# Kernel optimization log

Measured on AMD Instinct MI355X. Metric: run time of the kernel, lower is better.

## Reference

```python
import jax
import jax.numpy as jnp
from jax import lax
import numpy as np

N_PRE = 1024
N_POST = 2048
SEQ_LEN = 4096
DECAY = 0.9   # leak factor per timestep
V_TH = 1.0    # firing threshold


def setup_inputs() -> dict:
    key = jax.random.key(0)
    k1, k2 = jax.random.split(key)
    stim = (jax.random.uniform(k1, (N_PRE, SEQ_LEN), dtype=jnp.float32) < 0.1).astype(jnp.float32)  # sparse input spikes
    weights = jax.random.normal(k2, (N_POST, N_PRE), dtype=jnp.float32) * 0.05
    return {"stim": stim, "weights": weights}


def reference(stim, weights):
    # Synaptic currents for all timesteps at once: cal_post_input(stim[:, i]) == weights @ stim[:, i]
    currents = jnp.einsum("np,pt->nt", weights, stim)  # [n_post, T]

    def lif_step(v, i_t):
        # leaky integrate
        v = v * DECAY + i_t
        # fire
        s = (v >= V_TH).astype(v.dtype)
        # reset to 0 where spiked
        v_next = jnp.where(s > 0, jnp.zeros_like(v), v)
        return v_next, (s, v_next)

    v0 = jnp.zeros((N_POST,), dtype=stim.dtype)
    _, (spikes_t, v_t) = lax.scan(lif_step, v0, currents.T)  # scanned over T
    # transpose back to [n_post, T] to match spike_times / v buffers
    return spikes_t.T, v_t.T
```

## Files before the change

kernel.cpp:

```cpp
#include <hip/hip_runtime.h>

#define N_PRE 1024
#define N_POST 2048
#define SEQ_LEN 4096

#define KSPLIT 512

__device__ __forceinline__ float opaque(float x) {
  asm volatile("" : "+v"(x));
  return x;
}

__device__ __forceinline__ float load_dyn(const void* p, size_t idx, bool isbf) {
  if (isbf) {
    const unsigned short b = ((const unsigned short*)p)[idx];
    return __uint_as_float(((unsigned int)b) << 16);
  }
  return ((const float*)p)[idx];
}

__device__ __forceinline__ int sniff_flags(const void* W, const void* S, int tid,
                                           int* flags_sh) {
  if (tid < 64) {
    const unsigned short* uw = (const unsigned short*)W;
    const float f = fabsf(__uint_as_float(((unsigned int)uw[tid * 2]) << 16));
    const bool big = !(f < 64.f);
    const unsigned long long wb = __ballot(big);
    const unsigned short* us = (const unsigned short*)S;
    int hit = 0;
    for (int j = 0; j < 64; ++j) hit |= (us[tid * 128 + 2 * j] == 0x3F80u) ? 1 : 0;
    const unsigned long long sb = __ballot(hit != 0);
    if (tid == 0) *flags_sh = ((wb == 0ull) ? 1 : 0) | ((sb != 0ull) ? 2 : 0);
  }
  __syncthreads();
  return *flags_sh;
}

__global__ __launch_bounds__(256, 2) void snn_gemm_v2(const void* __restrict__ W,
                                                      const void* __restrict__ S,
                                                      float* __restrict__ C,
                                                      int t0, int chunkT) {
  __shared__ float As[16][132];
  __shared__ float Bs[16][132];
  __shared__ int flags_sh;
  const int tid = threadIdx.x;
  const int fl = sniff_flags(W, S, tid, &flags_sh);
  const bool w_bf = (fl & 1) != 0;
  const bool s_bf = (fl & 2) != 0;

  const int tx = tid & 15;
  const int ty = tid >> 4;
  const int m0 = blockIdx.y * 128;
  const int nl0 = blockIdx.x * 128;

  float acc0[8][8] = {{0.f}};
  float acc1[8][8] = {{0.f}};

  int k0 = 0;
#define KTILE_BODY(ACC)                                                          \
  {                                                                              \
                        \
    if (!w_bf) {                                                                 \
      const float* Wf = (const float*)W;                                         \
      const int row = tid >> 2;                                                  \
      const int c4 = (tid & 3) * 4;                                              \
      _Pragma("unroll") for (int h = 0; h < 2; ++h) {                            \
        const int m = row + 64 * h;                                              \
        const float4 va =                                                        \
            *(const float4*)&Wf[(size_t)(m0 + m) * N_PRE + k0 + c4];             \
        As[c4 + 0][m] = va.x; As[c4 + 1][m] = va.y;                              \
        As[c4 + 2][m] = va.z; As[c4 + 3][m] = va.w;                              \
      }                                                                          \
    } else {                                                                     \
      _Pragma("unroll") for (int e = 0; e < 8; ++e) {                            \
        const int idx = tid * 8 + e;                                             \
        const int m = idx >> 4, c = idx & 15;                                    \
        As[c][m] = load_dyn(W, (size_t)(m0 + m) * N_PRE + k0 + c, true);         \
      }                                                                          \
    }                                                                            \
                    \
    {                                                                            \
      const int r = tid >> 4;                                                    \
      const int c8 = (tid & 15) * 8;                                             \
      if (s_bf) {                                                                \
        const unsigned short* Sb = (const unsigned short*)S;                     \
        const uint4 u =                                                          \
            *(const uint4*)&Sb[(size_t)(k0 + r) * SEQ_LEN + t0 + nl0 + c8];      \
        Bs[r][c8 + 0] = __uint_as_float(u.x << 16);                              \
        Bs[r][c8 + 1] = __uint_as_float(u.x & 0xFFFF0000u);                      \
        Bs[r][c8 + 2] = __uint_as_float(u.y << 16);                              \
        Bs[r][c8 + 3] = __uint_as_float(u.y & 0xFFFF0000u);                      \
        Bs[r][c8 + 4] = __uint_as_float(u.z << 16);                              \
        Bs[r][c8 + 5] = __uint_as_float(u.z & 0xFFFF0000u);                      \
        Bs[r][c8 + 6] = __uint_as_float(u.w << 16);                              \
        Bs[r][c8 + 7] = __uint_as_float(u.w & 0xFFFF0000u);                      \
      } else {                                                                   \
        const float* Sf = (const float*)S;                                       \
        const size_t base = (size_t)(k0 + r) * SEQ_LEN + t0 + nl0 + c8;          \
        *(float4*)&Bs[r][c8] = *(const float4*)&Sf[base];                        \
        *(float4*)&Bs[r][c8 + 4] = *(const float4*)&Sf[base + 4];                \
      }                                                                          \
    }                                                                            \
    __syncthreads();                                                             \
    _Pragma("unroll") for (int k = 0; k < 16; ++k) {                             \
      float a[8], b[8];                                                          \
      *(float4*)&a[0] = *(const float4*)&As[k][ty * 8];                          \
      *(float4*)&a[4] = *(const float4*)&As[k][ty * 8 + 4];                      \
      *(float4*)&b[0] = *(const float4*)&Bs[k][tx * 8];                          \
      *(float4*)&b[4] = *(const float4*)&Bs[k][tx * 8 + 4];                      \
      _Pragma("unroll") for (int i = 0; i < 8; ++i)                              \
          _Pragma("unroll") for (int j = 0; j < 8; ++j)                          \
              ACC[i][j] += a[i] * b[j];       \
    }                                                                            \
    __syncthreads();                                                             \
  }

  for (; k0 < KSPLIT; k0 += 16) KTILE_BODY(acc0)
  for (; k0 < N_PRE; k0 += 16) KTILE_BODY(acc1)
#undef KTILE_BODY

#pragma unroll
  for (int i = 0; i < 8; ++i) {
    float r[8];
#pragma unroll
    for (int j = 0; j < 8; ++j) r[j] = acc0[i][j] + acc1[i][j];
    float* dst = &C[(size_t)(m0 + ty * 8 + i) * chunkT + nl0 + tx * 8];
    *(float4*)&dst[0] = make_float4(r[0], r[1], r[2], r[3]);
    *(float4*)&dst[4] = make_float4(r[4], r[5], r[6], r[7]);
  }
}

#define SROWS 16
#define STT 64
#define SPAD 68
__global__ __launch_bounds__(256) void snn_scan_v2(const float* __restrict__ cur,
                                                   float* __restrict__ spk,
                                                   float* __restrict__ vout,
                                                   float* __restrict__ v_carry,
                                                   int t0, int chunkT, int first) {
  __shared__ float c_t[2][SROWS][SPAD];
  __shared__ float s_t[SROWS][SPAD];
  __shared__ float v_t[SROWS][SPAD];
  const int tid = threadIdx.x;
  const int n0 = blockIdx.x * SROWS;
  const int row = tid >> 4;
  const int c4 = (tid & 15) * 4;

  float v = 0.0f;
  if (tid < SROWS && !first) v = v_carry[n0 + tid];

  const int ntiles = chunkT / STT;
  *(float4*)&c_t[0][row][c4] =
      *(const float4*)&cur[(size_t)(n0 + row) * chunkT + 0 + c4];
  __syncthreads();

  for (int it = 0; it < ntiles; ++it) {
    const int buf = it & 1;
    if (it + 1 < ntiles) {
      *(float4*)&c_t[buf ^ 1][row][c4] =
          *(const float4*)&cur[(size_t)(n0 + row) * chunkT + (it + 1) * STT + c4];
    }
    if (tid < SROWS) {
#pragma unroll
      for (int g = 0; g < STT / 16; ++g) {
        float c[16], s[16], vv[16];
        *(float4*)&c[0] = *(const float4*)&c_t[buf][tid][g * 16];
        *(float4*)&c[4] = *(const float4*)&c_t[buf][tid][g * 16 + 4];
        *(float4*)&c[8] = *(const float4*)&c_t[buf][tid][g * 16 + 8];
        *(float4*)&c[12] = *(const float4*)&c_t[buf][tid][g * 16 + 12];
#pragma unroll
        for (int k = 0; k < 16; ++k) {
          const float leak = opaque(v * 0.9f);
          v = leak + c[k];
          const bool fired = (v >= 1.0f);
          s[k] = fired ? 1.0f : 0.0f;
          v = fired ? 0.0f : v;
          vv[k] = v;
        }
        *(float4*)&s_t[tid][g * 16] = make_float4(s[0], s[1], s[2], s[3]);
        *(float4*)&s_t[tid][g * 16 + 4] = make_float4(s[4], s[5], s[6], s[7]);
        *(float4*)&s_t[tid][g * 16 + 8] = make_float4(s[8], s[9], s[10], s[11]);
        *(float4*)&s_t[tid][g * 16 + 12] = make_float4(s[12], s[13], s[14], s[15]);
        *(float4*)&v_t[tid][g * 16] = make_float4(vv[0], vv[1], vv[2], vv[3]);
        *(float4*)&v_t[tid][g * 16 + 4] = make_float4(vv[4], vv[5], vv[6], vv[7]);
        *(float4*)&v_t[tid][g * 16 + 8] = make_float4(vv[8], vv[9], vv[10], vv[11]);
        *(float4*)&v_t[tid][g * 16 + 12] = make_float4(vv[12], vv[13], vv[14], vv[15]);
      }
    }
    __syncthreads();
    {
      const size_t g = (size_t)(n0 + row) * SEQ_LEN + t0 + it * STT + c4;
      *(float4*)&spk[g] = *(const float4*)&s_t[row][c4];
      *(float4*)&vout[g] = *(const float4*)&v_t[row][c4];
    }
    __syncthreads();
  }

  if (tid < SROWS) v_carry[n0 + tid] = v;
}

__global__ __launch_bounds__(256) void snn_fused_blis(const void* __restrict__ W,
                                                      const void* __restrict__ S,
                                                      float* __restrict__ spk,
                                                      float* __restrict__ vout) {
  __shared__ float As[16][68];
  __shared__ float Bs[16][68];
  __shared__ float Ct[64][65];
  __shared__ float vsh[64];
  __shared__ int flags_sh;
  const int tid = threadIdx.x;
  const int fl = sniff_flags(W, S, tid, &flags_sh);
  const bool w_bf = (fl & 1) != 0;
  const bool s_bf = (fl & 2) != 0;

  const int tx = tid & 15;
  const int ty = tid >> 4;
  const int m0 = blockIdx.x * 64;
  if (tid < 64) vsh[tid] = 0.0f;

  for (int t0 = 0; t0 < SEQ_LEN; t0 += 64) {
    float acc0[4][4] = {{0.f}};
    float acc1[4][4] = {{0.f}};
    int k0 = 0;
#define FUSED_SEGMENT(ACC, KEND)                                                 \
    for (; k0 < (KEND); k0 += 16) {                                              \
      {                                                                          \
        const int r = tid >> 4, c = tid & 15;                                    \
        _Pragma("unroll") for (int j = 0; j < 4; ++j)                            \
            As[c][r + 16 * j] =                                                  \
                load_dyn(W, (size_t)(m0 + r + 16 * j) * N_PRE + k0 + c, w_bf);   \
      }                                                                          \
      {                                                                          \
        const int r = tid >> 6, c = tid & 63;                                    \
        _Pragma("unroll") for (int j = 0; j < 4; ++j)                            \
            Bs[r + 4 * j][c] =                                                   \
                load_dyn(S, (size_t)(k0 + r + 4 * j) * SEQ_LEN + t0 + c, s_bf);  \
      }                                                                          \
      __syncthreads();                                                           \
      _Pragma("unroll") for (int k = 0; k < 16; ++k) {                           \
        _Pragma("unroll") for (int i = 0; i < 4; ++i)                            \
            _Pragma("unroll") for (int j = 0; j < 4; ++j)                        \
                ACC[i][j] += As[k][ty * 4 + i] * Bs[k][tx * 4 + j];              \
      }                                                                          \
      __syncthreads();                                                           \
    }

    FUSED_SEGMENT(acc0, KSPLIT)
    FUSED_SEGMENT(acc1, N_PRE)
#undef FUSED_SEGMENT

#pragma unroll
    for (int i = 0; i < 4; ++i)
#pragma unroll
      for (int j = 0; j < 4; ++j) Ct[ty * 4 + i][tx * 4 + j] = acc0[i][j] + acc1[i][j];
    __syncthreads();
    if (tid < 64) {
      float v = vsh[tid];
#pragma unroll
      for (int k = 0; k < 64; ++k) {
        const float leak = opaque(v * 0.9f);
        v = leak + Ct[tid][k];
        const bool fired = (v >= 1.0f);
        const size_t g = (size_t)(m0 + tid) * SEQ_LEN + t0 + k;
        spk[g] = fired ? 1.0f : 0.0f;
        v = fired ? 0.0f : v;
        vout[g] = v;
      }
      vsh[tid] = v;
    }
    __syncthreads();
  }
}

extern "C" void kernel_launch(void* const* d_in, const int* in_sizes, int n_in,
                              void* d_out, int out_size, void* d_ws, size_t ws_size,
                              hipStream_t stream) {
  const void* stim = d_in[0];
  const void* weights = d_in[1];
  if (n_in >= 2 && in_sizes[0] == N_POST * N_PRE && in_sizes[1] == N_PRE * SEQ_LEN) {
    weights = d_in[0];
    stim = d_in[1];
  }

  float* spk = (float*)d_out;
  float* vout = spk + (size_t)N_POST * SEQ_LEN;

  const size_t carry_bytes = (size_t)N_POST * sizeof(float);
  float* v_carry = nullptr;
  size_t avail = 0;
  if (ws_size > carry_bytes + 8) {
    const size_t coff = (ws_size - carry_bytes) & ~(size_t)15;
    v_carry = (float*)((char*)d_ws + coff);
    avail = coff;
  }
  int chunkT = (int)((avail / ((size_t)N_POST * sizeof(float))) / 128 * 128);
  if (chunkT > SEQ_LEN) chunkT = SEQ_LEN;

  if (chunkT >= 128) {
    float* cur = (float*)d_ws;
    for (int t0 = 0; t0 < SEQ_LEN; t0 += chunkT) {
      const int ct = (SEQ_LEN - t0 < chunkT) ? (SEQ_LEN - t0) : chunkT;
      snn_gemm_v2<<<dim3(ct / 128, N_POST / 128), dim3(256), 0, stream>>>(weights, stim, cur,
                                                                          t0, ct);
      snn_scan_v2<<<dim3(N_POST / SROWS), dim3(256), 0, stream>>>(cur, spk, vout, v_carry,
                                                                  t0, ct, t0 == 0);
    }
  } else {
    snn_fused_blis<<<dim3(N_POST / 64), dim3(256), 0, stream>>>(weights, stim, spk, vout);
  }
}
```

Baseline: 410.9 us.

## Double-buffer GEMM tiles via register prefetch and shrink scan to single-wave blocks

The GEMM now keeps two LDS buffers and prefetches the next K-tile into registers while computing on the current one, which removes one barrier per tile. The B-fragment column mapping changes to strided halves to ease LDS bank conflicts. The scan kernel runs as a single 64-thread wave, so its __syncthreads calls can be dropped. Its recurrence is reordered to take the leak multiply off the critical dependency chain. Risks include more register pressure in the GEMM and reliance on implicit wave-level ordering of LDS accesses in the barrier-free scan.

Result: slower. 1.637 ms (+298.4%).

```diff
diff --git a/kernel.cpp b/kernel.cpp
--- a/kernel.cpp
+++ b/kernel.cpp
@@ -7,7 +7,7 @@
 #define KSPLIT 512
 
 __device__ __forceinline__ float opaque(float x) {
-  asm volatile("" : "+v"(x));
+  asm("" : "+v"(x));
   return x;
 }
 
@@ -36,12 +36,12 @@
   return *flags_sh;
 }
 
-__global__ __launch_bounds__(256, 2) void snn_gemm_v2(const void* __restrict__ W,
+__global__ __launch_bounds__(256, 2) void snn_gemm_v3(const void* __restrict__ W,
                                                       const void* __restrict__ S,
                                                       float* __restrict__ C,
                                                       int t0, int chunkT) {
-  __shared__ float As[16][132];
-  __shared__ float Bs[16][132];
+  __shared__ float As[2][16][132];
+  __shared__ float Bs[2][16][132];
   __shared__ int flags_sh;
   const int tid = threadIdx.x;
   const int fl = sniff_flags(W, S, tid, &flags_sh);
@@ -53,116 +53,157 @@
   const int m0 = blockIdx.y * 128;
   const int nl0 = blockIdx.x * 128;
 
+  const int arow = tid >> 2;
+  const int ac4 = (tid & 3) * 4;
+  const int br = tid >> 4;
+  const int bc8 = (tid & 15) * 8;
+
   float acc0[8][8] = {{0.f}};
   float acc1[8][8] = {{0.f}};
-
-  int k0 = 0;
-#define KTILE_BODY(ACC)                                                          \
+  float4 aR0, aR1;
+  uint4 bRa, bRb;
+
+#define GLOAD(KT)                                                                \
   {                                                                              \
-                        \
+    const int k0 = (KT) * 16;                                                    \
     if (!w_bf) {                                                                 \
       const float* Wf = (const float*)W;                                         \
-      const int row = tid >> 2;                                                  \
-      const int c4 = (tid & 3) * 4;                                              \
-      _Pragma("unroll") for (int h = 0; h < 2; ++h) {                            \
-        const int m = row + 64 * h;                                              \
-        const float4 va =                                                        \
-            *(const float4*)&Wf[(size_t)(m0 + m) * N_PRE + k0 + c4];             \
-        As[c4 + 0][m] = va.x; As[c4 + 1][m] = va.y;                              \
-        As[c4 + 2][m] = va.z; As[c4 + 3][m] = va.w;                              \
-      }                                                                          \
+      aR0 = *(const float4*)&Wf[(size_t)(m0 + arow) * N_PRE + k0 + ac4];         \
+      aR1 = *(const float4*)&Wf[(size_t)(m0 + arow + 64) * N_PRE + k0 + ac4];    \
+    }                                                                            \
+    if (s_bf) {                                                                  \
+      const unsigned short* Sb = (const unsigned short*)S;                       \
+      bRa = *(const uint4*)&Sb[(size_t)(k0 + br) * SEQ_LEN + t0 + nl0 + bc8];    \
     } else {                                                                     \
+      const float* Sf = (const float*)S;                                         \
+      const size_t base = (size_t)(k0 + br) * SEQ_LEN + t0 + nl0 + bc8;          \
+      bRa = *(const uint4*)&Sf[base];                                            \
+      bRb = *(const uint4*)&Sf[base + 4];                                        \
+    }                                                                            \
+  }
+
+#define LSTORE(BUF, KT)                                                          \
+  {                                                                              \
+    if (!w_bf) {                                                                 \
+      As[BUF][ac4 + 0][arow] = aR0.x; As[BUF][ac4 + 1][arow] = aR0.y;            \
+      As[BUF][ac4 + 2][arow] = aR0.z; As[BUF][ac4 + 3][arow] = aR0.w;            \
+      As[BUF][ac4 + 0][arow + 64] = aR1.x; As[BUF][ac4 + 1][arow + 64] = aR1.y;  \
+      As[BUF][ac4 + 2][arow + 64] = aR1.z; As[BUF][ac4 + 3][arow + 64] = aR1.w;  \
+    } else {                                                                     \
+      const int k0 = (KT) * 16;                                                  \
       _Pragma("unroll") for (int e = 0; e < 8; ++e) {                            \
         const int idx = tid * 8 + e;                                             \
         const int m = idx >> 4, c = idx & 15;                                    \
-        As[c][m] = load_dyn(W, (size_t)(m0 + m) * N_PRE + k0 + c, true);         \
+        As[BUF][c][m] = load_dyn(W, (size_t)(m0 + m) * N_PRE + k0 + c, true);    \
       }                                                                          \
     }                                                                            \
-                    \
-    {                                                                            \
-      const int r = tid >> 4;                                                    \
-      const int c8 = (tid & 15) * 8;                                             \
-      if (s_bf) {                                                                \
-        const unsigned short* Sb = (const unsigned short*)S;                     \
-        const uint4 u =                                                          \
-            *(const uint4*)&Sb[(size_t)(k0 + r) * SEQ_LEN + t0 + nl0 + c8];      \
-        Bs[r][c8 + 0] = __uint_as_float(u.x << 16);                              \
-        Bs[r][c8 + 1] = __uint_as_float(u.x & 0xFFFF0000u);                      \
-        Bs[r][c8 + 2] = __uint_as_float(u.y << 16);                              \
-        Bs[r][c8 + 3] = __uint_as_float(u.y & 0xFFFF0000u);                      \
-        Bs[r][c8 + 4] = __uint_as_float(u.z << 16);                              \
-        Bs[r][c8 + 5] = __uint_as_float(u.z & 0xFFFF0000u);                      \
-        Bs[r][c8 + 6] = __uint_as_float(u.w << 16);                              \
-        Bs[r][c8 + 7] = __uint_as_float(u.w & 0xFFFF0000u);                      \
-      } else {                                                                   \
-        const float* Sf = (const float*)S;                                       \
-        const size_t base = (size_t)(k0 + r) * SEQ_LEN + t0 + nl0 + c8;          \
-        *(float4*)&Bs[r][c8] = *(const float4*)&Sf[base];                        \
-        *(float4*)&Bs[r][c8 + 4] = *(const float4*)&Sf[base + 4];                \
-      }                                                                          \
-    }                                                                            \
-    __syncthreads();                                                             \
+    if (s_bf) {                                                                  \
+      float4 f0, f1;                                                             \
+      f0.x = __uint_as_float(bRa.x << 16);                                       \
+      f0.y = __uint_as_float(bRa.x & 0xFFFF0000u);                               \
+      f0.z = __uint_as_float(bRa.y << 16);                                       \
+      f0.w = __uint_as_float(bRa.y & 0xFFFF0000u);                               \
+      f1.x = __uint_as_float(bRa.z << 16);                                       \
+      f1.y = __uint_as_float(bRa.z & 0xFFFF0000u);                               \
+      f1.z = __uint_as_float(bRa.w << 16);                                       \
+      f1.w = __uint_as_float(bRa.w & 0xFFFF0000u);                               \
+      *(float4*)&Bs[BUF][br][bc8] = f0;                                          \
+      *(float4*)&Bs[BUF][br][bc8 + 4] = f1;                                      \
+    } else {                                                                     \
+      *(uint4*)&Bs[BUF][br][bc8] = bRa;                                          \
+      *(uint4*)&Bs[BUF][br][bc8 + 4] = bRb;                                      \
+    }                                                                            \
+  }
+
+#define COMPUTE(BUF, ACC)                                                        \
+  {                                                                              \
     _Pragma("unroll") for (int k = 0; k < 16; ++k) {                             \
       float a[8], b[8];                                                          \
-      *(float4*)&a[0] = *(const float4*)&As[k][ty * 8];                          \
-      *(float4*)&a[4] = *(const float4*)&As[k][ty * 8 + 4];                      \
-      *(float4*)&b[0] = *(const float4*)&Bs[k][tx * 8];                          \
-      *(float4*)&b[4] = *(const float4*)&Bs[k][tx * 8 + 4];                      \
+      *(float4*)&a[0] = *(const float4*)&As[BUF][k][ty * 8];                     \
+      *(float4*)&a[4] = *(const float4*)&As[BUF][k][ty * 8 + 4];                 \
+      *(float4*)&b[0] = *(const float4*)&Bs[BUF][k][tx * 4];        \
+      *(float4*)&b[4] = *(const float4*)&Bs[BUF][k][64 + tx * 4];   \
       _Pragma("unroll") for (int i = 0; i < 8; ++i)                              \
           _Pragma("unroll") for (int j = 0; j < 8; ++j)                          \
               ACC[i][j] += a[i] * b[j];       \
     }                                                                            \
+  }
+
+  GLOAD(0)
+  LSTORE(0, 0)
+  __syncthreads();
+
+  int kt = 0;
+#define STEP(ACC)                                                                \
+  {                                                                              \
+    const int buf = kt & 1;                                                      \
+    if (kt + 1 < 64) GLOAD(kt + 1)                                               \
+    COMPUTE(buf, ACC)                                                            \
+    if (kt + 1 < 64) LSTORE(buf ^ 1, kt + 1)                                     \
     __syncthreads();                                                             \
-  }
-
-  for (; k0 < KSPLIT; k0 += 16) KTILE_BODY(acc0)
-  for (; k0 < N_PRE; k0 += 16) KTILE_BODY(acc1)
-#undef KTILE_BODY
+    ++kt;                                                                        \
+  }
+
+  for (int i = 0; i < 32; ++i) STEP(acc0)
+  for (int i = 0; i < 32; ++i) STEP(acc1)
+#undef STEP
+#undef COMPUTE
+#undef LSTORE
+#undef GLOAD
 
 #pragma unroll
   for (int i = 0; i < 8; ++i) {
-    float r[8];
-#pragma unroll
-    for (int j = 0; j < 8; ++j) r[j] = acc0[i][j] + acc1[i][j];
-    float* dst = &C[(size_t)(m0 + ty * 8 + i) * chunkT + nl0 + tx * 8];
-    *(float4*)&dst[0] = make_float4(r[0], r[1], r[2], r[3]);
-    *(float4*)&dst[4] = make_float4(r[4], r[5], r[6], r[7]);
-  }
-}
-
-#define SROWS 16
+    float4 r0, r1;
+    r0.x = acc0[i][0] + acc1[i][0]; r0.y = acc0[i][1] + acc1[i][1];
+    r0.z = acc0[i][2] + acc1[i][2]; r0.w = acc0[i][3] + acc1[i][3];
+    r1.x = acc0[i][4] + acc1[i][4]; r1.y = acc0[i][5] + acc1[i][5];
+    r1.z = acc0[i][6] + acc1[i][6]; r1.w = acc0[i][7] + acc1[i][7];
+    float* dst = &C[(size_t)(m0 + ty * 8 + i) * chunkT + nl0 + tx * 4];
+    *(float4*)&dst[0] = r0;
+    *(float4*)&dst[64] = r1;
+  }
+}
+
 #define STT 64
-#define SPAD 68
-__global__ __launch_bounds__(256) void snn_scan_v2(const float* __restrict__ cur,
-                                                   float* __restrict__ spk,
-                                                   float* __restrict__ vout,
-                                                   float* __restrict__ v_carry,
-                                                   int t0, int chunkT, int first) {
-  __shared__ float c_t[2][SROWS][SPAD];
-  __shared__ float s_t[SROWS][SPAD];
-  __shared__ float v_t[SROWS][SPAD];
+__global__ __launch_bounds__(64) void snn_scan_v3(const float* __restrict__ cur,
+                                                  float* __restrict__ spk,
+                                                  float* __restrict__ vout,
+                                                  float* __restrict__ v_carry,
+                                                  int t0, int chunkT, int first) {
+  __shared__ float c_t[2][16][STT + 4];
+  __shared__ float s_t[16][STT + 4];
+  __shared__ float v_t[16][STT + 4];
   const int tid = threadIdx.x;
-  const int n0 = blockIdx.x * SROWS;
-  const int row = tid >> 4;
-  const int c4 = (tid & 15) * 4;
-
-  float v = 0.0f;
-  if (tid < SROWS && !first) v = v_carry[n0 + tid];
-
-  const int ntiles = chunkT / STT;
-  *(float4*)&c_t[0][row][c4] =
-      *(const float4*)&cur[(size_t)(n0 + row) * chunkT + 0 + c4];
-  __syncthreads();
-
-  for (int it = 0; it < ntiles; ++it) {
+  const int n0 = blockIdx.x * 16;
+  const int row = tid >> 2;
+  const int cq = (tid & 3) * 16;
+
+  float v0 = 0.0f;
+  if (tid < 16 && !first) v0 = v_carry[n0 + tid];
+  float leak = opaque(v0 * 0.9f);
+  float vpost = v0;
+
+  const int nt = chunkT / STT;
+  {
+    const float* src = &cur[(size_t)(n0 + row) * chunkT + cq];
+#pragma unroll
+    for (int u = 0; u < 4; ++u) *(float4*)&c_t[0][row][cq + 4 * u] = *(const float4*)&src[4 * u];
+  }
+
+  for (int it = 0; it < nt; ++it) {
     const int buf = it & 1;
-    if (it + 1 < ntiles) {
-      *(float4*)&c_t[buf ^ 1][row][c4] =
-          *(const float4*)&cur[(size_t)(n0 + row) * chunkT + (it + 1) * STT + c4];
-    }
-    if (tid < SROWS) {
-#pragma unroll
-      for (int g = 0; g < STT / 16; ++g) {
+    float4 p0, p1, p2, p3;
+    const bool pf = (it + 1 < nt);
+    if (pf) {
+      const float* src = &cur[(size_t)(n0 + row) * chunkT + (it + 1) * STT + cq];
+      p0 = *(const float4*)&src[0];
+      p1 = *(const float4*)&src[4];
+      p2 = *(const float4*)&src[8];
+      p3 = *(const float4*)&src[12];
+    }
+    if (tid < 16) {
+#pragma unroll
+      for (int g = 0; g < 4; ++g) {
         float c[16], s[16], vv[16];
         *(float4*)&c[0] = *(const float4*)&c_t[buf][tid][g * 16];
         *(float4*)&c[4] = *(const float4*)&c_t[buf][tid][g * 16 + 4];
@@ -170,12 +211,13 @@
         *(float4*)&c[12] = *(const float4*)&c_t[buf][tid][g * 16 + 12];
 #pragma unroll
         for (int k = 0; k < 16; ++k) {
-          const float leak = opaque(v * 0.9f);
-          v = leak + c[k];
-          const bool fired = (v >= 1.0f);
+          const float vpre = leak + c[k];
+          const bool fired = (vpre >= 1.0f);
+          const float m = opaque(vpre * 0.9f);
           s[k] = fired ? 1.0f : 0.0f;
-          v = fired ? 0.0f : v;
-          vv[k] = v;
+          vpost = fired ? 0.0f : vpre;
+          vv[k] = vpost;
+          leak = fired ? 0.0f : m;
         }
         *(float4*)&s_t[tid][g * 16] = make_float4(s[0], s[1], s[2], s[3]);
         *(float4*)&s_t[tid][g * 16 + 4] = make_float4(s[4], s[5], s[6], s[7]);
@@ -187,16 +229,23 @@
         *(float4*)&v_t[tid][g * 16 + 12] = make_float4(vv[12], vv[13], vv[14], vv[15]);
       }
     }
-    __syncthreads();
+    if (pf) {
+      *(float4*)&c_t[buf ^ 1][row][cq] = p0;
+      *(float4*)&c_t[buf ^ 1][row][cq + 4] = p1;
+      *(float4*)&c_t[buf ^ 1][row][cq + 8] = p2;
+      *(float4*)&c_t[buf ^ 1][row][cq + 12] = p3;
+    }
     {
-      const size_t g = (size_t)(n0 + row) * SEQ_LEN + t0 + it * STT + c4;
-      *(float4*)&spk[g] = *(const float4*)&s_t[row][c4];
-      *(float4*)&vout[g] = *(const float4*)&v_t[row][c4];
-    }
-    __syncthreads();
-  }
-
-  if (tid < SROWS) v_carry[n0 + tid] = v;
+      const size_t g = (size_t)(n0 + row) * SEQ_LEN + t0 + it * STT + cq;
+#pragma unroll
+      for (int u = 0; u < 4; ++u) {
+        *(float4*)&spk[g + 4 * u] = *(const float4*)&s_t[row][cq + 4 * u];
+        *(float4*)&vout[g + 4 * u] = *(const float4*)&v_t[row][cq + 4 * u];
+      }
+    }
+  }
+
+  if (tid < 16) v_carry[n0 + tid] = vpost;
 }
 
 __global__ __launch_bounds__(256) void snn_fused_blis(const void* __restrict__ W,
@@ -300,10 +349,10 @@
     float* cur = (float*)d_ws;
     for (int t0 = 0; t0 < SEQ_LEN; t0 += chunkT) {
       const int ct = (SEQ_LEN - t0 < chunkT) ? (SEQ_LEN - t0) : chunkT;
-      snn_gemm_v2<<<dim3(ct / 128, N_POST / 128), dim3(256), 0, stream>>>(weights, stim, cur,
+      snn_gemm_v3<<<dim3(ct / 128, N_POST / 128), dim3(256), 0, stream>>>(weights, stim, cur,
                                                                           t0, ct);
-      snn_scan_v2<<<dim3(N_POST / SROWS), dim3(256), 0, stream>>>(cur, spk, vout, v_carry,
-                                                                  t0, ct, t0 == 0);
+      snn_scan_v3<<<dim3(N_POST / 16), dim3(64), 0, stream>>>(cur, spk, vout, v_carry,
+                                                              t0, ct, t0 == 0);
     }
   } else {
     snn_fused_blis<<<dim3(N_POST / 64), dim3(256), 0, stream>>>(weights, stim, spk, vout);
```
